# Kernel tuning notes

Hardware: AMD Instinct MI355X
Metric: run time of the kernel (lower is better)

Reference implementation:

```python
import jax, jax.numpy as jnp
import numpy as np

B, S, D, H, E = 4, 2048, 1024, 4096, 8


def setup_inputs() -> dict:
    key = jax.random.key(0)
    ks = jax.random.split(key, 8)
    w = lambda k, shape: (jax.random.normal(k, shape, jnp.float32) * 0.02)
    return {
        "x": jax.random.normal(ks[0], (B, S, D), jnp.float32),
        "noise_eps": jax.random.normal(ks[1], (B, S, E), jnp.float32),
        "Wg": w(ks[2], (D, E)), "bg": jnp.zeros((E,), jnp.float32),
        "Wn": w(ks[3], (D, E)), "bn": jnp.zeros((E,), jnp.float32),
        "W1": w(ks[4], (E, D, H)), "b1": jnp.zeros((E, H), jnp.float32),
        "W2": w(ks[5], (E, H, D)), "b2": jnp.zeros((E, D), jnp.float32),
        "top_k": 2,
    }


def reference(x, noise_eps, Wg, bg, Wn, bn, W1, b1, W2, b2, top_k):
    b, s, d = x.shape
    e = Wg.shape[1]
    xt = x.reshape(-1, d)            # [T, D] flattened tokens
    eps = noise_eps.reshape(-1, e)   # [T, E]

    # Noisy top-k router
    logits = xt @ Wg + bg                                   # [T, E]
    noisy = logits + eps * jax.nn.softplus(xt @ Wn + bn)    # [T, E]
    top_vals, top_idx = jax.lax.top_k(noisy, top_k)         # [T, k]

    # sparse logits: -inf everywhere except top-k, then softmax -> 0 gate off-topk
    rows = jnp.arange(xt.shape[0])[:, None]
    sparse = jnp.full_like(noisy, -jnp.inf).at[rows, top_idx].set(top_vals)
    gate = jax.nn.softmax(sparse, axis=-1)                  # [T, E], zeros off-topk

    # Expert MLPs (exact GELU, as nn.GELU default); gate==0 off-topk reproduces
    # the masked gather/scatter combine of the original exactly.
    out = jnp.zeros_like(xt)
    for i in range(e):  # small fixed expert count
        h = jax.nn.gelu(xt @ W1[i] + b1[i], approximate=False)  # [T, H]
        o = h @ W2[i] + b2[i]                                   # [T, D]
        out = out + o * gate[:, i:i + 1]
    return out.reshape(b, s, d)
```

## Files before the change

kernel.cpp:

```cpp
#include <hip/hip_runtime.h>
#include <hip/hip_bf16.h>
#include <cmath>

#define T_TOK 8192
#define E_NUM 8
#define D_DIM 1024
#define H_DIM 4096

typedef __attribute__((ext_vector_type(4))) short bf16x4;
typedef __attribute__((ext_vector_type(8))) short bf16x8;
typedef __attribute__((ext_vector_type(4))) float f32x4;

__device__ __forceinline__ unsigned short f2bf(float f) {
  union { float f; unsigned u; } v; v.f = f;
  unsigned r = v.u + 0x7fffu + ((v.u >> 16) & 1u);
  return (unsigned short)(r >> 16);
}

__device__ __forceinline__ void gload_lds16(const void* g, void* l) {
  __builtin_amdgcn_global_load_lds(
      (const __attribute__((address_space(1))) unsigned int*)g,
      (__attribute__((address_space(3))) unsigned int*)l, 16, 0, 0);
}

__global__ void __launch_bounds__(256) cvt_x_kernel(const float* __restrict__ x,
                                                    ushort* __restrict__ xb) {
  int i = blockIdx.x * 256 + threadIdx.x;
  float4 v = ((const float4*)x)[i];
  ushort4 o;
  o.x = f2bf(v.x); o.y = f2bf(v.y); o.z = f2bf(v.z); o.w = f2bf(v.w);
  ((ushort4*)xb)[i] = o;
}

__global__ void __launch_bounds__(256) transpose_cvt_kernel(
    const float* __restrict__ src, ushort* __restrict__ dst, int K, int N) {
  __shared__ float tile[32][33];
  size_t eoff = (size_t)blockIdx.z * K * N;
  src += eoff; dst += eoff;
  int n0 = blockIdx.x * 32, k0 = blockIdx.y * 32;
  int tx = threadIdx.x & 31, ty = threadIdx.x >> 5;
  for (int i = 0; i < 32; i += 8)
    tile[ty + i][tx] = src[(size_t)(k0 + ty + i) * N + n0 + tx];
  __syncthreads();
  for (int i = 0; i < 32; i += 8)
    dst[(size_t)(n0 + ty + i) * K + k0 + tx] = f2bf(tile[tx][ty + i]);
}

__global__ void __launch_bounds__(256) router_kernel(
    const float* __restrict__ x, const float* __restrict__ eps,
    const float* __restrict__ Wg, const float* __restrict__ bg,
    const float* __restrict__ Wn, const float* __restrict__ bn,
    int* __restrict__ tok, float* __restrict__ gateL, int* __restrict__ cnt) {
  int lane = threadIdx.x & 63;
  int t = blockIdx.x * 4 + (threadIdx.x >> 6);
  float ag[8], an[8];
#pragma unroll
  for (int e = 0; e < 8; ++e) { ag[e] = 0.f; an[e] = 0.f; }
  const float* xr = x + (size_t)t * D_DIM;
#pragma unroll 4
  for (int i = 0; i < 16; ++i) {
    int d = lane + i * 64;
    float xv = xr[d];
    const float4* g4 = (const float4*)(Wg + d * 8);
    const float4* n4 = (const float4*)(Wn + d * 8);
    float4 ga = g4[0], gb = g4[1], na = n4[0], nb = n4[1];
    ag[0] += xv * ga.x; ag[1] += xv * ga.y; ag[2] += xv * ga.z; ag[3] += xv * ga.w;
    ag[4] += xv * gb.x; ag[5] += xv * gb.y; ag[6] += xv * gb.z; ag[7] += xv * gb.w;
    an[0] += xv * na.x; an[1] += xv * na.y; an[2] += xv * na.z; an[3] += xv * na.w;
    an[4] += xv * nb.x; an[5] += xv * nb.y; an[6] += xv * nb.z; an[7] += xv * nb.w;
  }
#pragma unroll
  for (int off = 32; off > 0; off >>= 1) {
#pragma unroll
    for (int e = 0; e < 8; ++e) {
      ag[e] += __shfl_xor(ag[e], off);
      an[e] += __shfl_xor(an[e], off);
    }
  }
  if (lane == 0) {
    float noisy[8];
#pragma unroll
    for (int e = 0; e < 8; ++e) {
      float lg = ag[e] + bg[e];
      float ln = an[e] + bn[e];
      float sp = (ln > 20.f) ? ln : log1pf(expf(ln));
      noisy[e] = lg + eps[(size_t)t * 8 + e] * sp;
    }
    int i0 = 0; float v0 = noisy[0];
#pragma unroll
    for (int e = 1; e < 8; ++e) if (noisy[e] > v0) { v0 = noisy[e]; i0 = e; }
    int i1 = -1; float v1 = -1e30f;
#pragma unroll
    for (int e = 0; e < 8; ++e) if (e != i0 && noisy[e] > v1) { v1 = noisy[e]; i1 = e; }
    float ee = expf(v1 - v0);
    float g0 = 1.f / (1.f + ee);
    float g1 = ee / (1.f + ee);
    int p0 = atomicAdd(cnt + i0, 1);
    int p1 = atomicAdd(cnt + i1, 1);
    tok[i0 * T_TOK + p0] = t * 2;     gateL[i0 * T_TOK + p0] = g0;
    tok[i1 * T_TOK + p1] = t * 2 + 1; gateL[i1 * T_TOK + p1] = g1;
  }
}

template <int KD, int NC, bool FIRST>
__global__ void __launch_bounds__(256) moe_gemm_kernel(
    const ushort* __restrict__ Abase, const ushort* __restrict__ Bt,
    const float* __restrict__ bias, const int* __restrict__ tok,
    const float* __restrict__ gateL, const int* __restrict__ cnt,
    ushort* __restrict__ hbuf, float* __restrict__ out) {
  constexpr int MT = T_TOK / 128;
  constexpr int NT = NC / 128;
  int nwg = MT * NT * E_NUM;
  int q = nwg >> 3;
  int bid = blockIdx.x;
  int wg = (bid & 7) * q + (bid >> 3);
  int m_t = wg % MT;
  int n_t = (wg / MT) % NT;
  int e = wg / (MT * NT);

  int c = cnt[e];
  int m0 = m_t * 128;
  if (m0 >= c) return;
  int n0 = n_t * 128;

  __shared__ __align__(16) ushort As[128 * 64];
  __shared__ __align__(16) ushort Bs[128 * 64];
  int tid = threadIdx.x;
  int lane = tid & 63, wave = tid >> 6;
  int wr = (wave >> 1) * 64, wc = (wave & 1) * 64;
  const int* tokE = tok + e * T_TOK;
  const ushort* Be = Bt + (size_t)e * NC * KD;

  int srow = tid >> 3, scol = tid & 7;
  const ushort* asrc[4]; const ushort* bsrc[4];
#pragma unroll
  for (int p = 0; p < 4; ++p) {
    int r = p * 32 + srow;
    int pi = m0 + r;
    int ar = 0;
    if (pi < c) { int tsv = tokE[pi]; ar = FIRST ? (tsv >> 1) : tsv; }
    int sl = (scol ^ (r & 7)) * 8;
    asrc[p] = Abase + (size_t)ar * KD + sl;
    bsrc[p] = Be + (size_t)(n0 + r) * KD + sl;
  }

  f32x4 acc[4][4];
#pragma unroll
  for (int i = 0; i < 4; ++i)
#pragma unroll
    for (int j = 0; j < 4; ++j) {
      f32x4 z = {0.f, 0.f, 0.f, 0.f};
      acc[i][j] = z;
    }

  int r16 = lane & 15;
  int kh8 = (lane >> 4) * 8;
  int swz = (r16 & 7) << 4;

  for (int kt = 0; kt < KD / 64; ++kt) {
    __syncthreads();
#pragma unroll
    for (int p = 0; p < 4; ++p)
      gload_lds16(asrc[p] + kt * 64, (char*)As + p * 4096 + tid * 16);
#pragma unroll
    for (int p = 0; p < 4; ++p)
      gload_lds16(bsrc[p] + kt * 64, (char*)Bs + p * 4096 + tid * 16);
    __syncthreads();

#pragma unroll
    for (int ks = 0; ks < 2; ++ks) {
      bf16x8 af[4], bfr[4];
      int k0 = ks * 64 + kh8;
#pragma unroll
      for (int i = 0; i < 4; ++i) {
        int rowA = (wr + i * 16 + r16) * 128;
        union { bf16x8 v8; bf16x4 v4[2]; } ua, ub;
        ua.v4[0] = *(const bf16x4*)((const char*)As + rowA + (k0 ^ swz));
        ua.v4[1] = *(const bf16x4*)((const char*)As + rowA + ((k0 + 32) ^ swz));
        af[i] = ua.v8;
        int rowB = (wc + i * 16 + r16) * 128;
        ub.v4[0] = *(const bf16x4*)((const char*)Bs + rowB + (k0 ^ swz));
        ub.v4[1] = *(const bf16x4*)((const char*)Bs + rowB + ((k0 + 32) ^ swz));
        bfr[i] = ub.v8;
      }
#pragma unroll
      for (int mi = 0; mi < 4; ++mi)
#pragma unroll
        for (int ni = 0; ni < 4; ++ni)
          acc[mi][ni] = __builtin_amdgcn_mfma_f32_16x16x32_bf16(
              af[mi], bfr[ni], acc[mi][ni], 0, 0, 0);
    }
  }

  const float* be = bias + (size_t)e * NC;
#pragma unroll
  for (int mi = 0; mi < 4; ++mi) {
#pragma unroll
    for (int r = 0; r < 4; ++r) {
      int rowl = wr + mi * 16 + ((lane >> 4) << 2) + r;
      int p = m0 + rowl;
      if (p < c) {
        int tsv = tokE[p];
        if (FIRST) {
          ushort* hrow = hbuf + (size_t)tsv * H_DIM;
#pragma unroll
          for (int ni = 0; ni < 4; ++ni) {
            int col = n0 + wc + ni * 16 + r16;
            float v = acc[mi][ni][r] + be[col];
            v = 0.5f * v * (1.f + erff(v * 0.70710678118654752f));
            hrow[col] = f2bf(v);
          }
        } else {
          float g = gateL[e * T_TOK + p];
          float* orow = out + (size_t)(tsv >> 1) * D_DIM;
#pragma unroll
          for (int ni = 0; ni < 4; ++ni) {
            int col = n0 + wc + ni * 16 + r16;
            float v = acc[mi][ni][r] + be[col];
            atomicAdd(&orow[col], g * v);
          }
        }
      }
    }
  }
}

extern "C" void kernel_launch(void* const* d_in, const int* in_sizes, int n_in,
                              void* d_out, int out_size, void* d_ws, size_t ws_size,
                              hipStream_t stream) {
  const float* x   = (const float*)d_in[0];
  const float* eps = (const float*)d_in[1];
  const float* Wg  = (const float*)d_in[2];
  const float* bg  = (const float*)d_in[3];
  const float* Wn  = (const float*)d_in[4];
  const float* bn  = (const float*)d_in[5];
  const float* W1  = (const float*)d_in[6];
  const float* b1  = (const float*)d_in[7];
  const float* W2  = (const float*)d_in[8];
  const float* b2  = (const float*)d_in[9];
  float* out = (float*)d_out;

  const size_t nXB = (size_t)T_TOK * D_DIM;
  const size_t nW1 = (size_t)E_NUM * D_DIM * H_DIM;
  const size_t nHB = (size_t)T_TOK * 2 * H_DIM;
  ushort* xb   = (ushort*)d_ws;
  ushort* W1T  = xb + nXB;
  ushort* W2T  = W1T + nW1;
  ushort* hbuf = W2T + nW1;
  int*   tok   = (int*)(hbuf + nHB);
  float* gateL = (float*)(tok + E_NUM * T_TOK);
  int*   cnt   = (int*)(gateL + E_NUM * T_TOK);
  size_t need = (size_t)((char*)(cnt + 8) - (char*)d_ws);
  if (ws_size < need) return;

  hipMemsetAsync(cnt, 0, 8 * sizeof(int), stream);
  hipMemsetAsync(out, 0, (size_t)out_size * sizeof(float), stream);

  cvt_x_kernel<<<(int)(nXB / 4 / 256), 256, 0, stream>>>(x, xb);
  transpose_cvt_kernel<<<dim3(H_DIM / 32, D_DIM / 32, E_NUM), 256, 0, stream>>>(
      W1, W1T, D_DIM, H_DIM);
  transpose_cvt_kernel<<<dim3(D_DIM / 32, H_DIM / 32, E_NUM), 256, 0, stream>>>(
      W2, W2T, H_DIM, D_DIM);
  router_kernel<<<T_TOK / 4, 256, 0, stream>>>(x, eps, Wg, bg, Wn, bn, tok, gateL, cnt);
  moe_gemm_kernel<D_DIM, H_DIM, true>
      <<<(T_TOK / 128) * (H_DIM / 128) * E_NUM, 256, 0, stream>>>(
          xb, W1T, b1, tok, gateL, cnt, hbuf, out);
  moe_gemm_kernel<H_DIM, D_DIM, false>
      <<<(T_TOK / 128) * (D_DIM / 128) * E_NUM, 256, 0, stream>>>(
          hbuf, W2T, b2, tok, gateL, cnt, hbuf, out);
}
```

Before: 1.131 ms.

## Permute K layout of operands so MFMA fragments load as single 16-byte LDS reads

Reorders the K dimension of the bf16 activations, transposed weights and the hidden buffer into a consistent permutation. Each lane can then fetch its bf16x8 MFMA fragment with one 16-byte LDS read instead of two 8-byte reads, using a new XOR swizzle. The weight transpose-convert kernel is also rewritten to use 64x64 tiles with float4 loads and 16-byte bf16 stores. The risk is correctness: every producer of A and B must apply the same K permutation, and the scattered 2-byte hbuf stores in the first GEMM epilogue get more awkward.

```diff
diff --git a/kernel.cpp b/kernel.cpp
--- a/kernel.cpp
+++ b/kernel.cpp
@@ -22,6 +22,7 @@
       (const __attribute__((address_space(1))) unsigned int*)g,
       (__attribute__((address_space(3))) unsigned int*)l, 16, 0, 0);
 }
+
 
 __global__ void __launch_bounds__(256) cvt_x_kernel(const float* __restrict__ x,
                                                     ushort* __restrict__ xb) {
@@ -29,21 +30,38 @@
   float4 v = ((const float4*)x)[i];
   ushort4 o;
   o.x = f2bf(v.x); o.y = f2bf(v.y); o.z = f2bf(v.z); o.w = f2bf(v.w);
-  ((ushort4*)xb)[i] = o;
+  int u = i & 7;
+  int oi = (i & ~7) | (((u & 3) << 1) | (u >> 2));
+  ((ushort4*)xb)[oi] = o;
 }
 
 __global__ void __launch_bounds__(256) transpose_cvt_kernel(
     const float* __restrict__ src, ushort* __restrict__ dst, int K, int N) {
-  __shared__ float tile[32][33];
+  __shared__ __align__(16) float tile[64][68];
   size_t eoff = (size_t)blockIdx.z * K * N;
-  src += eoff; dst += eoff;
-  int n0 = blockIdx.x * 32, k0 = blockIdx.y * 32;
-  int tx = threadIdx.x & 31, ty = threadIdx.x >> 5;
-  for (int i = 0; i < 32; i += 8)
-    tile[ty + i][tx] = src[(size_t)(k0 + ty + i) * N + n0 + tx];
+  int n0 = blockIdx.x * 64, k0 = blockIdx.y * 64;
+  int t = threadIdx.x;
+  int kr = t >> 4, nc = (t & 15) * 4;
+#pragma unroll
+  for (int i = 0; i < 4; ++i) {
+    float4 v = *(const float4*)(src + eoff + (size_t)(k0 + kr + i * 16) * N + n0 + nc);
+    *(float4*)&tile[kr + i * 16][nc] = v;
+  }
   __syncthreads();
-  for (int i = 0; i < 32; i += 8)
-    dst[(size_t)(n0 + ty + i) * K + k0 + tx] = f2bf(tile[tx][ty + i]);
+  int n = t >> 3, s = t & 7, g = s >> 2, p = s & 3;
+#pragma unroll
+  for (int j = 0; j < 2; ++j) {
+    int nn = n + j * 32;
+    union { bf16x8 v8; ushort e[8]; } o;
+#pragma unroll
+    for (int h = 0; h < 2; ++h)
+#pragma unroll
+      for (int r = 0; r < 4; ++r) {
+        int k = g * 32 + h * 16 + p * 4 + r;
+        o.e[h * 4 + r] = f2bf(tile[k][nn]);
+      }
+    *(bf16x8*)(dst + eoff + (size_t)(n0 + nn) * K + k0 + g * 32 + p * 8) = o.v8;
+  }
 }
 
 __global__ void __launch_bounds__(256) router_kernel(
@@ -111,9 +129,9 @@
   constexpr int MT = T_TOK / 128;
   constexpr int NT = NC / 128;
   int nwg = MT * NT * E_NUM;
-  int q = nwg >> 3;
+  int q8 = nwg >> 3;
   int bid = blockIdx.x;
-  int wg = (bid & 7) * q + (bid >> 3);
+  int wg = (bid & 7) * q8 + (bid >> 3);
   int m_t = wg % MT;
   int n_t = (wg / MT) % NT;
   int e = wg / (MT * NT);
@@ -154,8 +172,9 @@
     }
 
   int r16 = lane & 15;
-  int kh8 = (lane >> 4) * 8;
-  int swz = (r16 & 7) << 4;
+  int q = lane >> 4;
+  int rr = lane & 7;
+  int s0 = (q ^ rr) << 4;
 
   for (int kt = 0; kt < KD / 64; ++kt) {
     __syncthreads();
@@ -169,19 +188,12 @@
 
 #pragma unroll
     for (int ks = 0; ks < 2; ++ks) {
+      const int so = s0 ^ (ks << 6);
       bf16x8 af[4], bfr[4];
-      int k0 = ks * 64 + kh8;
 #pragma unroll
       for (int i = 0; i < 4; ++i) {
-        int rowA = (wr + i * 16 + r16) * 128;
-        union { bf16x8 v8; bf16x4 v4[2]; } ua, ub;
-        ua.v4[0] = *(const bf16x4*)((const char*)As + rowA + (k0 ^ swz));
-        ua.v4[1] = *(const bf16x4*)((const char*)As + rowA + ((k0 + 32) ^ swz));
-        af[i] = ua.v8;
-        int rowB = (wc + i * 16 + r16) * 128;
-        ub.v4[0] = *(const bf16x4*)((const char*)Bs + rowB + (k0 ^ swz));
-        ub.v4[1] = *(const bf16x4*)((const char*)Bs + rowB + ((k0 + 32) ^ swz));
-        bfr[i] = ub.v8;
+        af[i]  = *(const bf16x8*)((const char*)As + (wr + i * 16 + r16) * 128 + so);
+        bfr[i] = *(const bf16x8*)((const char*)Bs + (wc + i * 16 + r16) * 128 + so);
       }
 #pragma unroll
       for (int mi = 0; mi < 4; ++mi)
@@ -197,7 +209,7 @@
   for (int mi = 0; mi < 4; ++mi) {
 #pragma unroll
     for (int r = 0; r < 4; ++r) {
-      int rowl = wr + mi * 16 + ((lane >> 4) << 2) + r;
+      int rowl = wr + mi * 16 + q * 4 + r;
       int p = m0 + rowl;
       if (p < c) {
         int tsv = tokE[p];
@@ -208,7 +220,8 @@
             int col = n0 + wc + ni * 16 + r16;
             float v = acc[mi][ni][r] + be[col];
             v = 0.5f * v * (1.f + erff(v * 0.70710678118654752f));
-            hrow[col] = f2bf(v);
+            int pos = ((r16 >> 2) & 3) * 8 + (ni & 1) * 4 + (r16 & 3);
+            hrow[(col & ~31) + pos] = f2bf(v);
           }
         } else {
           float g = gateL[e * T_TOK + p];
@@ -257,9 +270,9 @@
   hipMemsetAsync(out, 0, (size_t)out_size * sizeof(float), stream);
 
   cvt_x_kernel<<<(int)(nXB / 4 / 256), 256, 0, stream>>>(x, xb);
-  transpose_cvt_kernel<<<dim3(H_DIM / 32, D_DIM / 32, E_NUM), 256, 0, stream>>>(
+  transpose_cvt_kernel<<<dim3(H_DIM / 64, D_DIM / 64, E_NUM), 256, 0, stream>>>(
       W1, W1T, D_DIM, H_DIM);
-  transpose_cvt_kernel<<<dim3(D_DIM / 32, H_DIM / 32, E_NUM), 256, 0, stream>>>(
+  transpose_cvt_kernel<<<dim3(D_DIM / 64, H_DIM / 64, E_NUM), 256, 0, stream>>>(
       W2, W2T, H_DIM, D_DIM);
   router_kernel<<<T_TOK / 4, 256, 0, stream>>>(x, eps, Wg, bg, Wn, bn, tok, gateL, cnt);
   moe_gemm_kernel<D_DIM, H_DIM, true>
```

Result: slower. 1.294 ms (+14.4%).
